# Kernel tuning notes

Hardware: AMD Instinct MI355X
Metric: run time of the kernel (lower is better)

## Reference

```python
import jax, jax.numpy as jnp
import numpy as np

B, S, D, H = 8, 2048, 1024, 64  # batch, seq, dimension, attention_head_size


def setup_inputs() -> dict:
    key = jax.random.key(0)
    k0, k1, k2, k3 = jax.random.split(key, 4)
    scale = 1.0 / np.sqrt(D)  # keep activations sane
    return {
        "x": jax.random.normal(k0, (B, S, D), dtype=jnp.float32),
        "Wq": jax.random.normal(k1, (D, H), dtype=jnp.float32) * scale,
        "Wk": jax.random.normal(k2, (D, H), dtype=jnp.float32) * scale,
        "Wv": jax.random.normal(k3, (D, H), dtype=jnp.float32) * scale,
    }


def reference(x, Wq, Wk, Wv):
    # Linear projections (bias=False); W stored as [D, H] == torch weight.T
    q = jnp.einsum("bsd,dh->bsh", x, Wq)
    k = jnp.einsum("bsd,dh->bsh", x, Wk)
    v = jnp.einsum("bsd,dh->bsh", x, Wv)
    # full score matrix, scaled by sqrt(head_size)
    scores = jnp.einsum("bqh,bkh->bqk", q, k) / jnp.sqrt(jnp.float32(H))
    weights = jax.nn.softmax(scores, axis=-1)  # [B, S, S]
    # dropout p=0.0 (eval): identity
    out = jnp.einsum("bqk,bkh->bqh", weights, v)  # [B, S, H]
    return out, weights
```

## Files before the change

kernel.cpp:

```cpp
#include <hip/hip_runtime.h>

#define SB 8
#define SS 2048
#define SD 1024
#define SH 64

typedef float f32x4 __attribute__((ext_vector_type(4)));
typedef __bf16 bf16x8 __attribute__((ext_vector_type(8)));

__device__ __forceinline__ unsigned short f2bf(float f) {
  union { float f; unsigned int u; } v; v.f = f;
  unsigned int u = v.u;
  unsigned int r = u + 0x7FFFu + ((u >> 16) & 1u);
  return (unsigned short)(r >> 16);
}

__global__ void prep_wt(const float* __restrict__ Wq, const float* __restrict__ Wk,
                        const float* __restrict__ Wv, unsigned short* __restrict__ Wt) {
  int idx = blockIdx.x * 256 + threadIdx.x;
  int hc = idx >> 10, d = idx & 1023;
  const float* W = (hc < 64) ? Wq : (hc < 128) ? Wk : Wv;
  int h = hc & 63;
  Wt[idx] = f2bf(W[d * SH + h]);
}

__global__ void __launch_bounds__(512, 2) proj(
    const float* __restrict__ x, const unsigned short* __restrict__ Wt,
    unsigned short* __restrict__ Q, unsigned short* __restrict__ K,
    unsigned short* __restrict__ Vt) {
  __shared__ unsigned short xs[64 * 64];
  __shared__ unsigned short Bl[2][192 * 64];

  int tid = threadIdx.x;
  int w = tid >> 6, lane = tid & 63;
  int l15 = lane & 15, kg = lane >> 4;
  int wr = w >> 2, wc = w & 3;
  int m0 = blockIdx.x * 64;

  int srow = tid >> 3, sseg = tid & 7;
  const float* xp = x + (size_t)(m0 + srow) * SD + sseg * 8;
  unsigned short* swp = xs + srow * 64 + ((sseg ^ (srow & 7)) * 8);

#define STAGEB(tt, buf)                                                          \
  {                                                                              \
    _Pragma("unroll") for (int j = 0; j < 3; ++j) {                              \
      int Lb = w * 1024 + j * 8192 + lane * 16;                                  \
      int c = Lb >> 7, cb = Lb & 127;                                            \
      const char* srcp = (const char*)Wt + (size_t)c * 2048 + (tt) * 128 +       \
                         (cb ^ ((c & 7) << 4));                                  \
      __builtin_amdgcn_global_load_lds(                                          \
          (const __attribute__((address_space(1))) unsigned int*)(const void*)srcp, \
          (__attribute__((address_space(3))) unsigned int*)(void*)                \
              ((char*)&Bl[(buf)][0] + w * 1024 + j * 8192),                      \
          16, 0, 0);                                                             \
    }                                                                            \
  }

  float4 ra = *(const float4*)xp;
  float4 rb = *(const float4*)(xp + 4);

  f32x4 acc[2][3];
#pragma unroll
  for (int mt = 0; mt < 2; ++mt)
#pragma unroll
    for (int nt = 0; nt < 3; ++nt) acc[mt][nt] = f32x4{0.f, 0.f, 0.f, 0.f};

  STAGEB(0, 0);

  for (int t = 0; t < 16; ++t) {
    union { unsigned short us[8]; bf16x8 v; } cv;
    cv.us[0] = f2bf(ra.x); cv.us[1] = f2bf(ra.y);
    cv.us[2] = f2bf(ra.z); cv.us[3] = f2bf(ra.w);
    cv.us[4] = f2bf(rb.x); cv.us[5] = f2bf(rb.y);
    cv.us[6] = f2bf(rb.z); cv.us[7] = f2bf(rb.w);
    *(bf16x8*)swp = cv.v;
    __syncthreads();

    if (t < 15) {
      STAGEB(t + 1, (t + 1) & 1);
      ra = *(const float4*)(xp + (t + 1) * 64);
      rb = *(const float4*)(xp + (t + 1) * 64 + 4);
    }

    const char* Bb = (const char*)&Bl[t & 1][0];
#pragma unroll
    for (int ks = 0; ks < 2; ++ks) {
      bf16x8 af[2];
#pragma unroll
      for (int mt = 0; mt < 2; ++mt) {
        int row = wr * 32 + mt * 16 + l15;
        int cg = ks * 4 + kg;
        af[mt] = *(const bf16x8*)(xs + row * 64 + ((cg ^ (row & 7)) * 8));
      }
#pragma unroll
      for (int nt = 0; nt < 3; ++nt) {
        int c = wc * 48 + nt * 16 + l15;
        int kb = (ks * 32 + kg * 8) * 2;
        bf16x8 bfr = *(const bf16x8*)(Bb + c * 128 + (kb ^ ((c & 7) << 4)));
#pragma unroll
        for (int mt = 0; mt < 2; ++mt)
          acc[mt][nt] = __builtin_amdgcn_mfma_f32_16x16x32_bf16(af[mt], bfr, acc[mt][nt], 0, 0, 0);
      }
    }
    __syncthreads();
  }

#pragma unroll
  for (int nt = 0; nt < 3; ++nt) {
    int c = wc * 48 + nt * 16 + l15;
    int mat = c >> 6, h = c & 63;
#pragma unroll
    for (int mt = 0; mt < 2; ++mt)
#pragma unroll
      for (int r = 0; r < 4; ++r) {
        int row = m0 + wr * 32 + mt * 16 + kg * 4 + r;
        unsigned short bv = f2bf(acc[mt][nt][r]);
        if (mat == 0) {
          Q[(size_t)row * SH + h] = bv;
        } else if (mat == 1) {
          K[(size_t)row * SH + h] = bv;
        } else {
          int bb = row >> 11, key = row & 2047;
          Vt[((size_t)bb * SH + h) * SS + key] = bv;
        }
      }
  }
}

__global__ void __launch_bounds__(512, 4) attn(
    const unsigned short* __restrict__ Q, const unsigned short* __restrict__ Kb,
    const unsigned short* __restrict__ Vt, float* __restrict__ out,
    float* __restrict__ wts) {
  __shared__ float pf[8][16][68];
  __shared__ float mS[8][16], sgS[8][16];

  int b = blockIdx.x & 7, rg = blockIdx.x >> 3;
  int w = threadIdx.x >> 6, lane = threadIdx.x & 63;
  int l15 = lane & 15, kg = lane >> 4;
  int q0 = rg * 16;
  int kv0 = w * 256;

  const unsigned short* Qb  = Q  + (size_t)b * SS * SH;
  const unsigned short* Kbb = Kb + (size_t)b * SS * SH;
  const unsigned short* Vtb = Vt + (size_t)b * SH * SS;

  bf16x8 qf[2];
#pragma unroll
  for (int ks = 0; ks < 2; ++ks)
    qf[ks] = *(const bf16x8*)(Qb + (size_t)(q0 + l15) * SH + ks * 32 + kg * 8);

  f32x4 s[4][4];
#pragma unroll
  for (int kt = 0; kt < 4; ++kt)
#pragma unroll
    for (int n = 0; n < 4; ++n) s[kt][n] = f32x4{0.f, 0.f, 0.f, 0.f};

  for (int kt = 0; kt < 4; ++kt) {
#pragma unroll
    for (int ks = 0; ks < 2; ++ks)
#pragma unroll
      for (int n = 0; n < 4; ++n) {
        bf16x8 kf = *(const bf16x8*)(Kbb + (size_t)(kv0 + kt * 64 + n * 16 + l15) * SH + ks * 32 + kg * 8);
        s[kt][n] = __builtin_amdgcn_mfma_f32_16x16x32_bf16(qf[ks], kf, s[kt][n], 0, 0, 0);
      }
  }

  float m[4], sg[4];
#pragma unroll
  for (int r = 0; r < 4; ++r) {
    float mloc = -1e30f;
#pragma unroll
    for (int kt = 0; kt < 4; ++kt)
#pragma unroll
      for (int n = 0; n < 4; ++n) mloc = fmaxf(mloc, s[kt][n][r]);
    mloc *= 0.125f;
#pragma unroll
    for (int off = 1; off < 16; off <<= 1) mloc = fmaxf(mloc, __shfl_xor(mloc, off));
    float ssum = 0.f;
#pragma unroll
    for (int kt = 0; kt < 4; ++kt)
#pragma unroll
      for (int n = 0; n < 4; ++n) {
        float e = __expf(s[kt][n][r] * 0.125f - mloc);
        s[kt][n][r] = e;
        ssum += e;
      }
#pragma unroll
    for (int off = 1; off < 16; off <<= 1) ssum += __shfl_xor(ssum, off);
    m[r] = mloc; sg[r] = ssum;
  }

  if (l15 == 0) {
#pragma unroll
    for (int r = 0; r < 4; ++r) {
      mS[w][kg * 4 + r] = m[r];
      sgS[w][kg * 4 + r] = sg[r];
    }
  }
  __syncthreads();

  float scal[4];
#pragma unroll
  for (int r = 0; r < 4; ++r) {
    int row = kg * 4 + r;
    float M = -1e30f;
#pragma unroll
    for (int ww = 0; ww < 8; ++ww) M = fmaxf(M, mS[ww][row]);
    float Sg = 0.f;
#pragma unroll
    for (int ww = 0; ww < 8; ++ww) Sg += sgS[ww][row] * __expf(mS[ww][row] - M);
    scal[r] = __expf(m[r] - M) / Sg;
  }

  float* wb = wts + (size_t)b * SS * SS;
  f32x4 oacc[4];
#pragma unroll
  for (int nh = 0; nh < 4; ++nh) oacc[nh] = f32x4{0.f, 0.f, 0.f, 0.f};

  for (int kt = 0; kt < 4; ++kt) {
#pragma unroll
    for (int n = 0; n < 4; ++n)
#pragma unroll
      for (int r = 0; r < 4; ++r)
        pf[w][kg * 4 + r][n * 16 + l15] = s[kt][n][r] * scal[r];
    asm volatile("s_waitcnt lgkmcnt(0)" ::: "memory");

#pragma unroll
    for (int i = 0; i < 4; ++i) {
      int row = i * 4 + kg;
      f32x4 pv4 = *(const f32x4*)&pf[w][row][l15 * 4];
      *(f32x4*)(wb + (size_t)(q0 + row) * SS + kv0 + kt * 64 + l15 * 4) = pv4;
    }

#pragma unroll
    for (int ks = 0; ks < 2; ++ks) {
      f32x4 pa = *(const f32x4*)&pf[w][l15][ks * 32 + kg * 8];
      f32x4 pb = *(const f32x4*)&pf[w][l15][ks * 32 + kg * 8 + 4];
      union { unsigned short us[8]; bf16x8 v; } pu;
#pragma unroll
      for (int i = 0; i < 4; ++i) { pu.us[i] = f2bf(pa[i]); pu.us[4 + i] = f2bf(pb[i]); }
#pragma unroll
      for (int nh = 0; nh < 4; ++nh) {
        bf16x8 vf = *(const bf16x8*)(Vtb + (size_t)(nh * 16 + l15) * SS + kv0 + kt * 64 + ks * 32 + kg * 8);
        oacc[nh] = __builtin_amdgcn_mfma_f32_16x16x32_bf16(pu.v, vf, oacc[nh], 0, 0, 0);
      }
    }
  }

#pragma unroll
  for (int nh = 0; nh < 4; ++nh)
#pragma unroll
    for (int r = 0; r < 4; ++r)
      pf[w][kg * 4 + r][nh * 16 + l15] = oacc[nh][r];
  __syncthreads();

  int tid = threadIdx.x;
#pragma unroll
  for (int half = 0; half < 2; ++half) {
    int e = tid + half * 512;
    int row = e >> 6, col = e & 63;
    float ssum = 0.f;
#pragma unroll
    for (int ww = 0; ww < 8; ++ww) ssum += pf[ww][row][col];
    out[((size_t)b * SS + q0 + row) * SH + col] = ssum;
  }
}

extern "C" void kernel_launch(void* const* d_in, const int* in_sizes, int n_in,
                              void* d_out, int out_size, void* d_ws, size_t ws_size,
                              hipStream_t stream) {
  const float* x  = (const float*)d_in[0];
  const float* Wq = (const float*)d_in[1];
  const float* Wk = (const float*)d_in[2];
  const float* Wv = (const float*)d_in[3];

  unsigned short* Wt = (unsigned short*)d_ws;
  unsigned short* Q  = Wt + 192 * 1024;
  unsigned short* K  = Q + 16384 * 64;
  unsigned short* Vt = K + 16384 * 64;

  float* out = (float*)d_out;
  float* wts = out + (size_t)SB * SS * SH;

  prep_wt<<<768, 256, 0, stream>>>(Wq, Wk, Wv, Wt);
  proj<<<256, 512, 0, stream>>>(x, Wt, Q, K, Vt);
  attn<<<1024, 512, 0, stream>>>(Q, K, Vt, out, wts);
}
```

Baseline: 98.98 us.

## Software-pipeline K loads in attention QK^T with inline asm and manual waitcnt

Replaces the compiler-scheduled K fragment loads in the score MFMA loop with inline-asm global_load_dwordx4 issued in double-buffered groups of four. Explicit s_waitcnt and sched_barrier calls overlap the next group's loads with the current group's MFMAs. The launch bounds are relaxed from 4 to 2 blocks per CU so the extra in-flight registers fit. The risks are lower occupancy and fragile manual vmcnt accounting, since the earlier Q loads also count toward vmcnt.

After: 101.1 us. 2.2% more time.

```diff
diff --git a/kernel.cpp b/kernel.cpp
--- a/kernel.cpp
+++ b/kernel.cpp
@@ -13,6 +13,10 @@
   unsigned int u = v.u;
   unsigned int r = u + 0x7FFFu + ((u >> 16) & 1u);
   return (unsigned short)(r >> 16);
+}
+
+__device__ __forceinline__ bf16x8 asbf(f32x4 x) {
+  union { f32x4 f; bf16x8 b; } u; u.f = x; return u.b;
 }
 
 __global__ void prep_wt(const float* __restrict__ Wq, const float* __restrict__ Wk,
@@ -127,7 +131,7 @@
   }
 }
 
-__global__ void __launch_bounds__(512, 4) attn(
+__global__ void __launch_bounds__(512, 2) attn(
     const unsigned short* __restrict__ Q, const unsigned short* __restrict__ Kb,
     const unsigned short* __restrict__ Vt, float* __restrict__ out,
     float* __restrict__ wts) {
@@ -144,10 +148,13 @@
   const unsigned short* Kbb = Kb + (size_t)b * SS * SH;
   const unsigned short* Vtb = Vt + (size_t)b * SH * SS;
 
-  bf16x8 qf[2];
-#pragma unroll
-  for (int ks = 0; ks < 2; ++ks)
-    qf[ks] = *(const bf16x8*)(Qb + (size_t)(q0 + l15) * SH + ks * 32 + kg * 8);
+  f32x4 qr0, qr1;
+  {
+    const unsigned short* qp0 = Qb + (size_t)(q0 + l15) * SH + kg * 8;
+    const unsigned short* qp1 = qp0 + 32;
+    asm volatile("global_load_dwordx4 %0, %1, off" : "=v"(qr0) : "v"(qp0));
+    asm volatile("global_load_dwordx4 %0, %1, off" : "=v"(qr1) : "v"(qp1));
+  }
 
   f32x4 s[4][4];
 #pragma unroll
@@ -155,15 +162,33 @@
 #pragma unroll
     for (int n = 0; n < 4; ++n) s[kt][n] = f32x4{0.f, 0.f, 0.f, 0.f};
 
-  for (int kt = 0; kt < 4; ++kt) {
-#pragma unroll
-    for (int ks = 0; ks < 2; ++ks)
-#pragma unroll
-      for (int n = 0; n < 4; ++n) {
-        bf16x8 kf = *(const bf16x8*)(Kbb + (size_t)(kv0 + kt * 64 + n * 16 + l15) * SH + ks * 32 + kg * 8);
-        s[kt][n] = __builtin_amdgcn_mfma_f32_16x16x32_bf16(qf[ks], kf, s[kt][n], 0, 0, 0);
-      }
-  }
+  f32x4 kA0, kA1, kA2, kA3, kB0, kB1, kB2, kB3;
+
+#define KADDR(KT, KS, N) \
+  (Kbb + (size_t)(kv0 + (KT) * 64 + (N) * 16 + l15) * SH + (KS) * 32 + kg * 8)
+#define KISSUE(S0, S1, S2, S3, KT, KS)                                            \
+  asm volatile("global_load_dwordx4 %0, %1, off" : "=v"(S0) : "v"(KADDR(KT, KS, 0))); \
+  asm volatile("global_load_dwordx4 %0, %1, off" : "=v"(S1) : "v"(KADDR(KT, KS, 1))); \
+  asm volatile("global_load_dwordx4 %0, %1, off" : "=v"(S2) : "v"(KADDR(KT, KS, 2))); \
+  asm volatile("global_load_dwordx4 %0, %1, off" : "=v"(S3) : "v"(KADDR(KT, KS, 3)));
+#define KWAIT(N)                              \
+  asm volatile("s_waitcnt vmcnt(" #N ")");    \
+  __builtin_amdgcn_sched_barrier(0);
+#define KMFMA(S0, S1, S2, S3, KT, KS)                                                     \
+  s[KT][0] = __builtin_amdgcn_mfma_f32_16x16x32_bf16((KS) ? asbf(qr1) : asbf(qr0), asbf(S0), s[KT][0], 0, 0, 0); \
+  s[KT][1] = __builtin_amdgcn_mfma_f32_16x16x32_bf16((KS) ? asbf(qr1) : asbf(qr0), asbf(S1), s[KT][1], 0, 0, 0); \
+  s[KT][2] = __builtin_amdgcn_mfma_f32_16x16x32_bf16((KS) ? asbf(qr1) : asbf(qr0), asbf(S2), s[KT][2], 0, 0, 0); \
+  s[KT][3] = __builtin_amdgcn_mfma_f32_16x16x32_bf16((KS) ? asbf(qr1) : asbf(qr0), asbf(S3), s[KT][3], 0, 0, 0);
+
+  KISSUE(kA0, kA1, kA2, kA3, 0, 0);
+  KISSUE(kB0, kB1, kB2, kB3, 0, 1); KWAIT(4); KMFMA(kA0, kA1, kA2, kA3, 0, 0);
+  KISSUE(kA0, kA1, kA2, kA3, 1, 0); KWAIT(4); KMFMA(kB0, kB1, kB2, kB3, 0, 1);
+  KISSUE(kB0, kB1, kB2, kB3, 1, 1); KWAIT(4); KMFMA(kA0, kA1, kA2, kA3, 1, 0);
+  KISSUE(kA0, kA1, kA2, kA3, 2, 0); KWAIT(4); KMFMA(kB0, kB1, kB2, kB3, 1, 1);
+  KISSUE(kB0, kB1, kB2, kB3, 2, 1); KWAIT(4); KMFMA(kA0, kA1, kA2, kA3, 2, 0);
+  KISSUE(kA0, kA1, kA2, kA3, 3, 0); KWAIT(4); KMFMA(kB0, kB1, kB2, kB3, 2, 1);
+  KISSUE(kB0, kB1, kB2, kB3, 3, 1); KWAIT(4); KMFMA(kA0, kA1, kA2, kA3, 3, 0);
+                                    KWAIT(0); KMFMA(kB0, kB1, kB2, kB3, 3, 1);
 
   float m[4], sg[4];
 #pragma unroll
```

## Halve projection row tile to 32 and double-buffer the x tile

Applied to the files above, without the earlier changes.

The projection kernel now handles 32 rows per block instead of 64, so the grid grows from 256 to 512 blocks and the 256 CUs are better occupied. The x tile in shared memory is double-buffered, and the next tile's bf16 conversion and store are overlapped with the MFMAs on the current one, which removes one barrier per iteration. The cost is that the weight tile is now streamed twice as often in total, and each wave does half the MFMA work per B fragment it loads.

New measurement: 93.01 us. -6.0%, faster.

```diff
diff --git a/kernel.cpp b/kernel.cpp
--- a/kernel.cpp
+++ b/kernel.cpp
@@ -28,18 +28,18 @@
     const float* __restrict__ x, const unsigned short* __restrict__ Wt,
     unsigned short* __restrict__ Q, unsigned short* __restrict__ K,
     unsigned short* __restrict__ Vt) {
-  __shared__ unsigned short xs[64 * 64];
+  __shared__ unsigned short xs[2][32 * 64];
   __shared__ unsigned short Bl[2][192 * 64];
 
   int tid = threadIdx.x;
   int w = tid >> 6, lane = tid & 63;
   int l15 = lane & 15, kg = lane >> 4;
   int wr = w >> 2, wc = w & 3;
-  int m0 = blockIdx.x * 64;
-
-  int srow = tid >> 3, sseg = tid & 7;
-  const float* xp = x + (size_t)(m0 + srow) * SD + sseg * 8;
-  unsigned short* swp = xs + srow * 64 + ((sseg ^ (srow & 7)) * 8);
+  int m0 = blockIdx.x * 32;
+
+  int srow = tid >> 4, sseg = tid & 15;
+  const float* xp = x + (size_t)(m0 + srow) * SD + sseg * 4;
+  int swoff = srow * 64 + (((sseg >> 1) ^ (srow & 7)) << 3) + ((sseg & 1) << 2);
 
 #define STAGEB(tt, buf)                                                          \
   {                                                                              \
@@ -56,50 +56,42 @@
     }                                                                            \
   }
 
+#define CVTW(RA, buf)                                                           \
+  {                                                                             \
+    ushort4 cv;                                                                 \
+    cv.x = f2bf((RA).x); cv.y = f2bf((RA).y);                                   \
+    cv.z = f2bf((RA).z); cv.w = f2bf((RA).w);                                   \
+    *(ushort4*)(&xs[(buf)][0] + swoff) = cv;                                    \
+  }
+
+  f32x4 acc[3];
+#pragma unroll
+  for (int nt = 0; nt < 3; ++nt) acc[nt] = f32x4{0.f, 0.f, 0.f, 0.f};
+
   float4 ra = *(const float4*)xp;
-  float4 rb = *(const float4*)(xp + 4);
-
-  f32x4 acc[2][3];
-#pragma unroll
-  for (int mt = 0; mt < 2; ++mt)
-#pragma unroll
-    for (int nt = 0; nt < 3; ++nt) acc[mt][nt] = f32x4{0.f, 0.f, 0.f, 0.f};
-
   STAGEB(0, 0);
+  CVTW(ra, 0);
+  ra = *(const float4*)(xp + 64);
+  __syncthreads();
 
   for (int t = 0; t < 16; ++t) {
-    union { unsigned short us[8]; bf16x8 v; } cv;
-    cv.us[0] = f2bf(ra.x); cv.us[1] = f2bf(ra.y);
-    cv.us[2] = f2bf(ra.z); cv.us[3] = f2bf(ra.w);
-    cv.us[4] = f2bf(rb.x); cv.us[5] = f2bf(rb.y);
-    cv.us[6] = f2bf(rb.z); cv.us[7] = f2bf(rb.w);
-    *(bf16x8*)swp = cv.v;
-    __syncthreads();
-
-    if (t < 15) {
-      STAGEB(t + 1, (t + 1) & 1);
-      ra = *(const float4*)(xp + (t + 1) * 64);
-      rb = *(const float4*)(xp + (t + 1) * 64 + 4);
-    }
-
-    const char* Bb = (const char*)&Bl[t & 1][0];
+    int cur = t & 1, nxt = (t + 1) & 1;
+    if (t < 15) CVTW(ra, nxt);
+    if (t < 14) ra = *(const float4*)(xp + (t + 2) * 64);
+    if (t < 15) STAGEB(t + 1, nxt);
+
+    const char* Bb = (const char*)&Bl[cur][0];
 #pragma unroll
     for (int ks = 0; ks < 2; ++ks) {
-      bf16x8 af[2];
-#pragma unroll
-      for (int mt = 0; mt < 2; ++mt) {
-        int row = wr * 32 + mt * 16 + l15;
-        int cg = ks * 4 + kg;
-        af[mt] = *(const bf16x8*)(xs + row * 64 + ((cg ^ (row & 7)) * 8));
-      }
+      int row = wr * 16 + l15;
+      int cg = ks * 4 + kg;
+      bf16x8 af = *(const bf16x8*)(&xs[cur][0] + row * 64 + ((cg ^ (row & 7)) << 3));
 #pragma unroll
       for (int nt = 0; nt < 3; ++nt) {
         int c = wc * 48 + nt * 16 + l15;
         int kb = (ks * 32 + kg * 8) * 2;
         bf16x8 bfr = *(const bf16x8*)(Bb + c * 128 + (kb ^ ((c & 7) << 4)));
-#pragma unroll
-        for (int mt = 0; mt < 2; ++mt)
-          acc[mt][nt] = __builtin_amdgcn_mfma_f32_16x16x32_bf16(af[mt], bfr, acc[mt][nt], 0, 0, 0);
+        acc[nt] = __builtin_amdgcn_mfma_f32_16x16x32_bf16(af, bfr, acc[nt], 0, 0, 0);
       }
     }
     __syncthreads();
@@ -110,20 +102,18 @@
     int c = wc * 48 + nt * 16 + l15;
     int mat = c >> 6, h = c & 63;
 #pragma unroll
-    for (int mt = 0; mt < 2; ++mt)
-#pragma unroll
-      for (int r = 0; r < 4; ++r) {
-        int row = m0 + wr * 32 + mt * 16 + kg * 4 + r;
-        unsigned short bv = f2bf(acc[mt][nt][r]);
-        if (mat == 0) {
-          Q[(size_t)row * SH + h] = bv;
-        } else if (mat == 1) {
-          K[(size_t)row * SH + h] = bv;
-        } else {
-          int bb = row >> 11, key = row & 2047;
-          Vt[((size_t)bb * SH + h) * SS + key] = bv;
-        }
-      }
+    for (int r = 0; r < 4; ++r) {
+      int row = m0 + wr * 16 + kg * 4 + r;
+      unsigned short bv = f2bf(acc[nt][r]);
+      if (mat == 0) {
+        Q[(size_t)row * SH + h] = bv;
+      } else if (mat == 1) {
+        K[(size_t)row * SH + h] = bv;
+      } else {
+        int bb = row >> 11, key = row & 2047;
+        Vt[((size_t)bb * SH + h) * SS + key] = bv;
+      }
+    }
   }
 }
 
@@ -283,6 +273,6 @@
   float* wts = out + (size_t)SB * SS * SH;
 
   prep_wt<<<768, 256, 0, stream>>>(Wq, Wk, Wv, Wt);
-  proj<<<256, 512, 0, stream>>>(x, Wt, Q, K, Vt);
+  proj<<<512, 512, 0, stream>>>(x, Wt, Q, K, Vt);
   attn<<<1024, 512, 0, stream>>>(Q, K, Vt, out, wts);
 }
```
